# Performance work log

Measured on AMD Instinct MI355X. Metric: run time of the kernel, lower is better.

## Reference

```python
import jax, jax.numpy as jnp
import numpy as np

B, N_NODE, FN, FE = 8, 128, 64, 64  # batch, n_node, n_node_fea, n_edge_fea


def setup_inputs() -> dict:
    key = jax.random.key(0)
    k = jax.random.split(key, 7)
    stdv_w = 1.0 / np.sqrt(2 * FN + FE)  # torch reset uses 1/sqrt(size(0))
    stdv_b = 1.0 / np.sqrt(FN)
    return {
        "H": jax.random.normal(k[0], (B, N_NODE, FN), jnp.float32),
        "A": jax.random.uniform(k[1], (B, N_NODE, N_NODE), jnp.float32),
        "E": jax.random.normal(k[2], (B, N_NODE, N_NODE, FE), jnp.float32),
        "W_att": jax.random.uniform(k[3], (2 * FN + FE, FN), jnp.float32, -stdv_w, stdv_w),
        "W_nei": jax.random.uniform(k[4], (2 * FN + FE, FN), jnp.float32, -stdv_w, stdv_w),
        "bias_att": jax.random.uniform(k[5], (FN,), jnp.float32, -stdv_b, stdv_b),
        "bias_nei": jax.random.uniform(k[6], (FN,), jnp.float32, -stdv_b, stdv_b),
        "N": N_NODE,
    }


def _branch(H, A, E, W, bias, fn):
    # (A[...,None] * cat(H_i, H_j, E)) @ W + bias, computed without
    # materializing the [B,N,N,2F+Fe] concat: split W into row blocks.
    f = H.shape[-1]
    Wi, Wj, We = W[:f], W[f:2 * f], W[2 * f:]
    proj = (
        jnp.einsum('bif,fl->bil', H, Wi)[:, :, None, :]   # H_i broadcast over j
        + jnp.einsum('bjf,fl->bjl', H, Wj)[:, None, :, :] # H_j broadcast over i
        + jnp.einsum('bije,el->bijl', E, We)
    )
    return A[..., None] * proj + bias  # [B, N, N, F]


def reference(H, A, E, W_att, W_nei, bias_att, bias_nei, N):
    att = _branch(H, A, E, W_att, bias_att, None)
    conv = _branch(H, A, E, W_nei, bias_nei, None)
    gated = jax.nn.sigmoid(att) * jax.nn.relu(conv)  # [B, N, N, F]
    return jnp.sum(gated, axis=1)  # sum over first node axis -> [B, N, F]
```

## Files before the change

kernel.cpp:

```cpp
#include <hip/hip_runtime.h>


typedef _Float16 half8 __attribute__((ext_vector_type(8)));
typedef float floatx4 __attribute__((ext_vector_type(4)));

__device__ __forceinline__ half8 cvt2(const float4 a, const float4 b) {
  half8 v;
  v[0] = (_Float16)a.x; v[1] = (_Float16)a.y; v[2] = (_Float16)a.z; v[3] = (_Float16)a.w;
  v[4] = (_Float16)b.x; v[5] = (_Float16)b.y; v[6] = (_Float16)b.z; v[7] = (_Float16)b.w;
  return v;
}

__global__ __launch_bounds__(256, 2)
void amp_fused(const float* __restrict__ H, const float* __restrict__ A,
               const float* __restrict__ E,
               const float* __restrict__ Wa, const float* __restrict__ Wn,
               const float* __restrict__ ba, const float* __restrict__ bn,
               float* __restrict__ out) {
  const int bx = blockIdx.x;
  const int b = bx >> 6;
  const int rem = bx & 63;
  const int jt = rem >> 3;
  const int ch = rem & 7;
  const int w = threadIdx.x >> 6;
  const int lane = threadIdx.x & 63;
  const int quad = lane >> 4;
  const int l15 = lane & 15;
  const int i0b = ch * 16;
  const int i0 = i0b + w * 4;
  const int j0 = jt * 16;
  const float* Wptr[2] = {Wa, Wn};

  half8 hi[2], hj[2];
  {
    const float* hib = H + (b * 128 + i0b + l15) * 64 + quad * 8;
    const float* hjb = H + (b * 128 + j0 + l15) * 64 + quad * 8;
#pragma unroll
    for (int hh = 0; hh < 2; ++hh) {
      hi[hh] = cvt2(*reinterpret_cast<const float4*>(hib + hh * 32),
                    *reinterpret_cast<const float4*>(hib + hh * 32 + 4));
      hj[hh] = cvt2(*reinterpret_cast<const float4*>(hjb + hh * 32),
                    *reinterpret_cast<const float4*>(hjb + hh * 32 + 4));
    }
  }

  float pia_all[2][4][4];
  float pj[2][4][4];
  for (int br = 0; br < 2; ++br) {
    const float* W = Wptr[br];
#pragma unroll
    for (int t = 0; t < 4; ++t) {
      floatx4 z = {0.f, 0.f, 0.f, 0.f};
      floatx4 pif = z, pjf = z;
#pragma unroll
      for (int hh = 0; hh < 2; ++hh) {
        const float* wi = W + (hh * 32 + quad * 8) * 64 + t * 16 + l15;
        const float* wj = W + (64 + hh * 32 + quad * 8) * 64 + t * 16 + l15;
        half8 bi, bj;
#pragma unroll
        for (int x = 0; x < 8; ++x) { bi[x] = (_Float16)wi[x * 64]; bj[x] = (_Float16)wj[x * 64]; }
        pif = __builtin_amdgcn_mfma_f32_16x16x32_f16(hi[hh], bi, pif, 0, 0, 0);
        pjf = __builtin_amdgcn_mfma_f32_16x16x32_f16(hj[hh], bj, pjf, 0, 0, 0);
      }
#pragma unroll
      for (int r = 0; r < 4; ++r) pj[br][t][r] = pjf[r];
#pragma unroll
      for (int ii = 0; ii < 4; ++ii)
        pia_all[br][t][ii] = __shfl(pif[ii], w * 16 + l15);
    }
  }

  half8 wf[2][4][2];
#pragma unroll
  for (int br = 0; br < 2; ++br)
#pragma unroll
    for (int t = 0; t < 4; ++t)
#pragma unroll
      for (int hh = 0; hh < 2; ++hh) {
        const float* wsrc = Wptr[br] + (128 + hh * 32 + quad * 8) * 64 + t * 16 + l15;
        half8 v;
#pragma unroll
        for (int x = 0; x < 8; ++x) v[x] = (_Float16)wsrc[x * 64];
        wf[br][t][hh] = v;
      }

  float biasv[2][4];
#pragma unroll
  for (int t = 0; t < 4; ++t) {
    biasv[0][t] = ba[t * 16 + l15];
    biasv[1][t] = bn[t * 16 + l15];
  }

  float acc[4][4];
#pragma unroll
  for (int t = 0; t < 4; ++t)
#pragma unroll
    for (int r = 0; r < 4; ++r) acc[t][r] = 0.f;

#pragma unroll
  for (int ii = 0; ii < 4; ++ii) {
    const int i = i0 + ii;
    const float* erow = E + ((size_t)((b * 128 + i) * 128 + j0 + l15)) * 64 + quad * 8;
    half8 a0 = cvt2(*reinterpret_cast<const float4*>(erow),
                    *reinterpret_cast<const float4*>(erow + 4));
    half8 a1 = cvt2(*reinterpret_cast<const float4*>(erow + 32),
                    *reinterpret_cast<const float4*>(erow + 36));

    const float4 av4 = *reinterpret_cast<const float4*>(
        A + (b * 128 + i) * 128 + j0 + quad * 4);
    const float av[4] = {av4.x, av4.y, av4.z, av4.w};

#pragma unroll
    for (int t = 0; t < 4; ++t) {
      floatx4 z = {0.f, 0.f, 0.f, 0.f};
      floatx4 pa = __builtin_amdgcn_mfma_f32_16x16x32_f16(a0, wf[0][t][0], z, 0, 0, 0);
      pa = __builtin_amdgcn_mfma_f32_16x16x32_f16(a1, wf[0][t][1], pa, 0, 0, 0);
      floatx4 pn = __builtin_amdgcn_mfma_f32_16x16x32_f16(a0, wf[1][t][0], z, 0, 0, 0);
      pn = __builtin_amdgcn_mfma_f32_16x16x32_f16(a1, wf[1][t][1], pn, 0, 0, 0);
#pragma unroll
      for (int r = 0; r < 4; ++r) {
        float att = av[r] * (pa[r] + pia_all[0][t][ii] + pj[0][t][r]) + biasv[0][t];
        float cnv = av[r] * (pn[r] + pia_all[1][t][ii] + pj[1][t][r]) + biasv[1][t];
        float ex = __expf(-att);
        float sig = __builtin_amdgcn_rcpf(1.0f + ex);
        acc[t][r] += sig * fmaxf(cnv, 0.f);
      }
    }
  }

  __shared__ float red[4][16][64];
#pragma unroll
  for (int t = 0; t < 4; ++t)
#pragma unroll
    for (int r = 0; r < 4; ++r)
      red[w][quad * 4 + r][t * 16 + l15] = acc[t][r];
  __syncthreads();

  const int tid = threadIdx.x;
#pragma unroll
  for (int k = 0; k < 4; ++k) {
    int idx = k * 256 + tid;
    int jl = idx >> 6;
    int l = idx & 63;
    float s = red[0][jl][l] + red[1][jl][l] + red[2][jl][l] + red[3][jl][l];
    atomicAdd(out + (b * 128 + j0 + jl) * 64 + l, s);
  }
}

extern "C" void kernel_launch(void* const* d_in, const int* in_sizes, int n_in,
                              void* d_out, int out_size, void* d_ws, size_t ws_size,
                              hipStream_t stream) {
  const float* H = (const float*)d_in[0];
  const float* A = (const float*)d_in[1];
  const float* E = (const float*)d_in[2];
  const float* Wa = (const float*)d_in[3];
  const float* Wn = (const float*)d_in[4];
  const float* ba = (const float*)d_in[5];
  const float* bn = (const float*)d_in[6];
  float* out = (float*)d_out;

  hipMemsetAsync(d_out, 0, (size_t)out_size * sizeof(float), stream);
  amp_fused<<<512, 256, 0, stream>>>(H, A, E, Wa, Wn, ba, bn, out);
}
```

Before: 101.4 us.

## Stage converted weight fragments in LDS and split node projections across waves

Each block now converts all W fragments to fp16 once into shared memory, with every wave doing a twelfth-share of the strided global loads, instead of every wave reloading and converting them all. The H_i/H_j projection MFMAs are also divided among the four waves and exchanged through LDS rather than computed redundantly by each wave. This cuts redundant strided global reads and conversions in the prologue. In exchange it uses a 48KB shared buffer, which may limit occupancy, and adds several block barriers.

```diff
diff --git a/kernel.cpp b/kernel.cpp
--- a/kernel.cpp
+++ b/kernel.cpp
@@ -31,6 +31,12 @@
   const int j0 = jt * 16;
   const float* Wptr[2] = {Wa, Wn};
 
+  __shared__ __align__(16) char smem[48 * 1024];
+  _Float16* fraglds = reinterpret_cast<_Float16*>(smem);
+  float* pflds = reinterpret_cast<float*>(smem);
+  float* pjlds = reinterpret_cast<float*>(smem + 8 * 1024);
+  float (*red)[16][64] = reinterpret_cast<float (*)[16][64]>(smem);
+
   half8 hi[2], hj[2];
   {
     const float* hib = H + (b * 128 + i0b + l15) * 64 + quad * 8;
@@ -44,45 +50,64 @@
     }
   }
 
+#pragma unroll
+  for (int k = 0; k < 12; ++k) {
+    const int F = w * 12 + k;
+    const int kind = F >> 4;
+    const int f = F & 15;
+    const int br = f >> 3;
+    const int t = (f >> 1) & 3;
+    const int hh = f & 1;
+    const float* src = Wptr[br] + (kind * 64 + hh * 32 + quad * 8) * 64 + t * 16 + l15;
+    half8 v;
+#pragma unroll
+    for (int x = 0; x < 8; ++x) v[x] = (_Float16)src[x * 64];
+    *reinterpret_cast<half8*>(fraglds + F * 512 + lane * 8) = v;
+  }
+  __syncthreads();
+
+  floatx4 pif[2], pjf[2];
+#pragma unroll
+  for (int pp = 0; pp < 2; ++pp) {
+    const int p = w * 2 + pp;
+    const int br = p >> 2;
+    const int t = p & 3;
+    floatx4 z = {0.f, 0.f, 0.f, 0.f};
+    pif[pp] = z; pjf[pp] = z;
+#pragma unroll
+    for (int hh = 0; hh < 2; ++hh) {
+      half8 bi = *reinterpret_cast<half8*>(fraglds + (br * 8 + t * 2 + hh) * 512 + lane * 8);
+      half8 bj = *reinterpret_cast<half8*>(fraglds + (16 + br * 8 + t * 2 + hh) * 512 + lane * 8);
+      pif[pp] = __builtin_amdgcn_mfma_f32_16x16x32_f16(hi[hh], bi, pif[pp], 0, 0, 0);
+      pjf[pp] = __builtin_amdgcn_mfma_f32_16x16x32_f16(hj[hh], bj, pjf[pp], 0, 0, 0);
+    }
+  }
+  __syncthreads();
+#pragma unroll
+  for (int pp = 0; pp < 2; ++pp) {
+    const int p = w * 2 + pp;
+    *reinterpret_cast<floatx4*>(pflds + (p * 64 + lane) * 4) = pif[pp];
+    *reinterpret_cast<floatx4*>(pjlds + (p * 64 + lane) * 4) = pjf[pp];
+  }
+  __syncthreads();
+
   float pia_all[2][4][4];
   float pj[2][4][4];
-  for (int br = 0; br < 2; ++br) {
-    const float* W = Wptr[br];
-#pragma unroll
-    for (int t = 0; t < 4; ++t) {
-      floatx4 z = {0.f, 0.f, 0.f, 0.f};
-      floatx4 pif = z, pjf = z;
-#pragma unroll
-      for (int hh = 0; hh < 2; ++hh) {
-        const float* wi = W + (hh * 32 + quad * 8) * 64 + t * 16 + l15;
-        const float* wj = W + (64 + hh * 32 + quad * 8) * 64 + t * 16 + l15;
-        half8 bi, bj;
-#pragma unroll
-        for (int x = 0; x < 8; ++x) { bi[x] = (_Float16)wi[x * 64]; bj[x] = (_Float16)wj[x * 64]; }
-        pif = __builtin_amdgcn_mfma_f32_16x16x32_f16(hi[hh], bi, pif, 0, 0, 0);
-        pjf = __builtin_amdgcn_mfma_f32_16x16x32_f16(hj[hh], bj, pjf, 0, 0, 0);
-      }
-#pragma unroll
-      for (int r = 0; r < 4; ++r) pj[br][t][r] = pjf[r];
-#pragma unroll
-      for (int ii = 0; ii < 4; ++ii)
-        pia_all[br][t][ii] = __shfl(pif[ii], w * 16 + l15);
-    }
-  }
-
   half8 wf[2][4][2];
 #pragma unroll
   for (int br = 0; br < 2; ++br)
 #pragma unroll
-    for (int t = 0; t < 4; ++t)
+    for (int t = 0; t < 4; ++t) {
+      const int p = br * 4 + t;
+      const floatx4 pjv = *reinterpret_cast<const floatx4*>(pjlds + (p * 64 + lane) * 4);
+      const floatx4 piv = *reinterpret_cast<const floatx4*>(pflds + (p * 64 + w * 16 + l15) * 4);
 #pragma unroll
-      for (int hh = 0; hh < 2; ++hh) {
-        const float* wsrc = Wptr[br] + (128 + hh * 32 + quad * 8) * 64 + t * 16 + l15;
-        half8 v;
+      for (int r = 0; r < 4; ++r) { pj[br][t][r] = pjv[r]; pia_all[br][t][r] = piv[r]; }
 #pragma unroll
-        for (int x = 0; x < 8; ++x) v[x] = (_Float16)wsrc[x * 64];
-        wf[br][t][hh] = v;
-      }
+      for (int hh = 0; hh < 2; ++hh)
+        wf[br][t][hh] = *reinterpret_cast<half8*>(
+            fraglds + (32 + br * 8 + t * 2 + hh) * 512 + lane * 8);
+    }
 
   float biasv[2][4];
 #pragma unroll
@@ -128,7 +153,7 @@
     }
   }
 
-  __shared__ float red[4][16][64];
+  __syncthreads();
 #pragma unroll
   for (int t = 0; t < 4; ++t)
 #pragma unroll
```

Result: faster. 97.46 us (-3.9%).
